# Optimization experiments

Measured on AMD Instinct MI355X. Metric: run time of the kernel, lower is better.

Reference implementation:

```python
import jax, jax.numpy as jnp
import numpy as np

FP8_MAX = 448.0  # max representable magnitude of float8_e4m3fn
SCALE_EPS = 1e-7


def setup_inputs() -> dict:
    key = jax.random.key(0)
    k1, k2, k3 = jax.random.split(key, 3)
    in_f, out_f = 2048, 2048
    x = jax.random.normal(k1, (4, 4096, in_f), dtype=jnp.float32)
    # weight is stored in fp8 in the torch module; materialize fp8-representable fp32 values
    w_fp32 = jax.random.normal(k2, (out_f, in_f), dtype=jnp.float32) * (1.0 / np.sqrt(in_f))
    weight = w_fp32.astype(jnp.float8_e4m3fn).astype(jnp.float32)
    weight_scale = jnp.ones((), dtype=jnp.float32)
    bound = 1.0 / np.sqrt(in_f)
    bias = jax.random.uniform(k3, (out_f,), dtype=jnp.float32, minval=-bound, maxval=bound)
    return {"x": x, "weight": weight, "weight_scale": weight_scale, "bias": bias}


def reference(x, weight, weight_scale, bias):
    # per-tensor dynamic fp8 quantization of the input (scale = absmax / 448)
    scale = jnp.maximum(jnp.max(jnp.abs(x)) / FP8_MAX, SCALE_EPS)
    x_q = (x / scale).astype(jnp.float8_e4m3fn).astype(jnp.float32)
    # dequantize weight (fp8 values stored as fp32 here) with its per-tensor scale
    w = weight * weight_scale
    # NOTE: faithful to the source, the output is NOT rescaled by the input scale
    # (the original forward drops input_scale after quantization).
    out = jnp.einsum('bsi,oi->bso', x_q, w) + bias
    return out
```

## Files before the change

### kernel.cpp

```cpp
#include <hip/hip_runtime.h>
#include <hip/hip_bf16.h>

typedef __attribute__((ext_vector_type(4))) float floatx4;
typedef __attribute__((ext_vector_type(8))) int   intx8;

#define FP8_MAX_F 448.0f
#define SCALE_EPS 1e-7f

__global__ void k_pre(const float* __restrict__ x, unsigned* __restrict__ amax, int n4,
                      const float* __restrict__ w, int* __restrict__ wq, int nw16) {
    if (blockIdx.x < 1792) {
        __shared__ float wmax[4];
        int tid = blockIdx.x * 256 + threadIdx.x;
        int stride = 1792 * 256;
        const float4* x4 = (const float4*)x;
        float m = 0.f;
        for (int i = tid; i < n4; i += stride) {
            float4 v = x4[i];
            m = fmaxf(fmaxf(fabsf(v.x), fabsf(v.y)),
                      fmaxf(m, fmaxf(fabsf(v.z), fabsf(v.w))));
        }
        #pragma unroll
        for (int off = 32; off > 0; off >>= 1) m = fmaxf(m, __shfl_xor(m, off, 64));
        if ((threadIdx.x & 63) == 0) wmax[threadIdx.x >> 6] = m;
        __syncthreads();
        if (threadIdx.x == 0) {
            float t = fmaxf(fmaxf(wmax[0], wmax[1]), fmaxf(wmax[2], wmax[3]));
            atomicMax(amax, __float_as_uint(t));
        }
    } else {
        int tid = (blockIdx.x - 1792) * 256 + threadIdx.x;
        int stride = 256 * 256;
        const float4* x4 = (const float4*)w;
        int4* q4 = (int4*)wq;
        for (int i = tid; i < nw16; i += stride) {
            float4 v0 = x4[4*i], v1 = x4[4*i+1], v2 = x4[4*i+2], v3 = x4[4*i+3];
            int4 o;
            o.x = __builtin_amdgcn_cvt_pk_fp8_f32(v0.x, v0.y, 0, false);
            o.x = __builtin_amdgcn_cvt_pk_fp8_f32(v0.z, v0.w, o.x, true);
            o.y = __builtin_amdgcn_cvt_pk_fp8_f32(v1.x, v1.y, 0, false);
            o.y = __builtin_amdgcn_cvt_pk_fp8_f32(v1.z, v1.w, o.y, true);
            o.z = __builtin_amdgcn_cvt_pk_fp8_f32(v2.x, v2.y, 0, false);
            o.z = __builtin_amdgcn_cvt_pk_fp8_f32(v2.z, v2.w, o.z, true);
            o.w = __builtin_amdgcn_cvt_pk_fp8_f32(v3.x, v3.y, 0, false);
            o.w = __builtin_amdgcn_cvt_pk_fp8_f32(v3.z, v3.w, o.w, true);
            q4[i] = o;
        }
    }
}

__global__ void k_quant_x(const float* __restrict__ x, int* __restrict__ xq,
                          const unsigned* __restrict__ amax, int n16) {
    float scale = fmaxf(__uint_as_float(*amax) / FP8_MAX_F, SCALE_EPS);
    int tid = blockIdx.x * blockDim.x + threadIdx.x;
    int stride = gridDim.x * blockDim.x;
    const float4* x4 = (const float4*)x;
    int4* q4 = (int4*)xq;
    for (int i = tid; i < n16; i += stride) {
        float4 v0 = x4[4*i], v1 = x4[4*i+1], v2 = x4[4*i+2], v3 = x4[4*i+3];
        int4 o;
        o.x = __builtin_amdgcn_cvt_pk_fp8_f32(v0.x / scale, v0.y / scale, 0, false);
        o.x = __builtin_amdgcn_cvt_pk_fp8_f32(v0.z / scale, v0.w / scale, o.x, true);
        o.y = __builtin_amdgcn_cvt_pk_fp8_f32(v1.x / scale, v1.y / scale, 0, false);
        o.y = __builtin_amdgcn_cvt_pk_fp8_f32(v1.z / scale, v1.w / scale, o.y, true);
        o.z = __builtin_amdgcn_cvt_pk_fp8_f32(v2.x / scale, v2.y / scale, 0, false);
        o.z = __builtin_amdgcn_cvt_pk_fp8_f32(v2.z / scale, v2.w / scale, o.z, true);
        o.w = __builtin_amdgcn_cvt_pk_fp8_f32(v3.x / scale, v3.y / scale, 0, false);
        o.w = __builtin_amdgcn_cvt_pk_fp8_f32(v3.z / scale, v3.w / scale, o.w, true);
        q4[i] = o;
    }
}

#define BM 256
#define BN 256
#define BKQ 128
#define NT 16

#define GLOAD(src, dst) \
    __builtin_amdgcn_global_load_lds((const __attribute__((address_space(1))) void*)(src), \
                                     (__attribute__((address_space(3))) void*)(dst), 16, 0, 0)
#define BARRIER()   asm volatile("s_barrier" ::: "memory")
#define WAIT_VM(n)  asm volatile("s_waitcnt vmcnt(" #n ")" ::: "memory")

#define LDFRAG(dstv, pL, pH, IMM) {                      \
    int4 lo_ = *(const int4*)((pL) + (IMM));             \
    int4 hi_ = *(const int4*)((pH) + (IMM));             \
    dstv = (intx8){lo_.x, lo_.y, lo_.z, lo_.w, hi_.x, hi_.y, hi_.z, hi_.w}; }

#define MFMA_ROW(m, af)                                                            \
    acc[m][0] = __builtin_amdgcn_mfma_scale_f32_16x16x128_f8f6f4(                  \
        af, b0, acc[m][0], 0, 0, 0, 0x7F7F7F7F, 0, 0x7F7F7F7F);                    \
    acc[m][1] = __builtin_amdgcn_mfma_scale_f32_16x16x128_f8f6f4(                  \
        af, b1, acc[m][1], 0, 0, 0, 0x7F7F7F7F, 0, 0x7F7F7F7F);                    \
    acc[m][2] = __builtin_amdgcn_mfma_scale_f32_16x16x128_f8f6f4(                  \
        af, b2, acc[m][2], 0, 0, 0, 0x7F7F7F7F, 0, 0x7F7F7F7F);                    \
    acc[m][3] = __builtin_amdgcn_mfma_scale_f32_16x16x128_f8f6f4(                  \
        af, b3, acc[m][3], 0, 0, 0, 0x7F7F7F7F, 0, 0x7F7F7F7F);

__global__ __launch_bounds__(512, 2) void k_gemm_mx(
    const unsigned char* __restrict__ A, const unsigned char* __restrict__ B,
    const float* __restrict__ bias, const float* __restrict__ wscale,
    float* __restrict__ C, int M, int N, int K) {
    __shared__ __align__(16) unsigned char lds[131072];

    int nwg = gridDim.x;
    int bid = blockIdx.x;
    bid = (bid & 7) * (nwg >> 3) + (bid >> 3);
    int ntn = N / BN;
    int tm = bid / ntn, tn = bid % ntn;
    int row0 = tm * BM, col0 = tn * BN;

    int tid = (int)threadIdx.x;
    int lane = tid & 63, wid = tid >> 6;
    int wr = wid >> 2, wc = wid & 3;
    int fr = lane & 15, g = lane >> 4;

    int srow = tid >> 3;
    int sc   = (tid & 7) ^ (srow & 7);
    const int offA0 = (row0 + srow) * K + sc * 16;
    const int offB0 = (col0 + srow) * K + sc * 16;
    unsigned char* dstA = lds + tid * 16;
    unsigned char* dstB = dstA + 32768;

    int c0 = (2 * g) ^ (fr & 7);
    const int aL = wr * 16384 + fr * 128 + c0 * 16;
    const int aH = wr * 16384 + fr * 128 + (c0 ^ 1) * 16;
    const int bL = 32768 + wc * 8192 + fr * 128 + c0 * 16;
    const int bH = 32768 + wc * 8192 + fr * 128 + (c0 ^ 1) * 16;

    floatx4 acc[8][4];
    #pragma unroll
    for (int m = 0; m < 8; ++m)
        #pragma unroll
        for (int n = 0; n < 4; ++n) acc[m][n] = (floatx4)(0.f);

    GLOAD(A + offA0,          dstA);
    GLOAD(A + offA0 + 131072, dstA + 8192);
    GLOAD(A + offA0 + 262144, dstA + 16384);
    GLOAD(A + offA0 + 393216, dstA + 24576);
    GLOAD(B + offB0,          dstB);
    GLOAD(B + offB0 + 131072, dstB + 8192);
    GLOAD(B + offB0 + 262144, dstB + 16384);
    GLOAD(B + offB0 + 393216, dstB + 24576);

    for (int t = 0; t < NT; ++t) {
        const int bufo = (t & 1) << 16;
        const int nbufo = bufo ^ 65536;
        const unsigned char* AbL = lds + bufo + aL;
        const unsigned char* AbH = lds + bufo + aH;
        const unsigned char* BbL = lds + bufo + bL;
        const unsigned char* BbH = lds + bufo + bH;
        unsigned char* dA = dstA + nbufo;
        unsigned char* dB = dstB + nbufo;
        const int kn = ((t + 1) & (NT - 1)) * BKQ;

        GLOAD(A + kn + offA0,          dA);
        GLOAD(A + kn + offA0 + 131072, dA + 8192);
        GLOAD(A + kn + offA0 + 262144, dA + 16384);
        GLOAD(A + kn + offA0 + 393216, dA + 24576);
        GLOAD(B + kn + offB0,          dB);
        GLOAD(B + kn + offB0 + 131072, dB + 8192);
        GLOAD(B + kn + offB0 + 262144, dB + 16384);
        GLOAD(B + kn + offB0 + 393216, dB + 24576);
        WAIT_VM(8);
        BARRIER();

        intx8 b0, b1, b2, b3, a0, a1, a2, a3, a4, a5, a6, a7;
        LDFRAG(b0, BbL, BbH, 0)
        LDFRAG(b1, BbL, BbH, 2048)
        LDFRAG(b2, BbL, BbH, 4096)
        LDFRAG(b3, BbL, BbH, 6144)
        LDFRAG(a0, AbL, AbH, 0)
        LDFRAG(a1, AbL, AbH, 2048)
        LDFRAG(a2, AbL, AbH, 4096)
        LDFRAG(a3, AbL, AbH, 6144)
        LDFRAG(a4, AbL, AbH, 8192)
        LDFRAG(a5, AbL, AbH, 10240)
        LDFRAG(a6, AbL, AbH, 12288)
        LDFRAG(a7, AbL, AbH, 14336)
        MFMA_ROW(0, a0)
        MFMA_ROW(1, a1)
        MFMA_ROW(2, a2)
        MFMA_ROW(3, a3)
        MFMA_ROW(4, a4)
        MFMA_ROW(5, a5)
        MFMA_ROW(6, a6)
        MFMA_ROW(7, a7)
        BARRIER();
    }

    WAIT_VM(0);

    float wsv = *wscale;
    int crow = (lane >> 4) * 4;
    int ccol = lane & 15;
    float bv[4];
    #pragma unroll
    for (int n = 0; n < 4; ++n) bv[n] = bias[col0 + wc * 64 + n * 16 + ccol];
    #pragma unroll
    for (int m = 0; m < 8; ++m) {
        int r = row0 + wr * 128 + m * 16 + crow;
        #pragma unroll
        for (int n = 0; n < 4; ++n) {
            int c = col0 + wc * 64 + n * 16 + ccol;
            #pragma unroll
            for (int j = 0; j < 4; ++j)
                C[(long)(r + j) * N + c] = acc[m][n][j] * wsv + bv[n];
        }
    }
}

extern "C" void kernel_launch(void* const* d_in, const int* in_sizes, int n_in,
                              void* d_out, int out_size, void* d_ws, size_t ws_size,
                              hipStream_t stream) {
    const float* x      = (const float*)d_in[0];
    const float* w      = (const float*)d_in[1];
    const float* wscale = (const float*)d_in[2];
    const float* bias   = (const float*)d_in[3];
    float* out = (float*)d_out;

    const int K = 2048, N = 2048;
    const int M = in_sizes[0] / K;

    unsigned char* ws = (unsigned char*)d_ws;
    unsigned* amax = (unsigned*)ws;
    int* wq = (int*)(ws + 1024);
    int* xq = (int*)(ws + 1024 + (size_t)N * K);

    hipMemsetAsync(amax, 0, 4, stream);
    k_pre<<<2048, 256, 0, stream>>>(x, amax, (M * K) / 4, w, wq, (N * K) / 16);
    k_quant_x<<<2048, 256, 0, stream>>>(x, xq, amax, (M * K) / 16);

    int grid = (M / BM) * (N / BN);
    k_gemm_mx<<<grid, 512, 0, stream>>>((const unsigned char*)xq, (const unsigned char*)wq,
                                        bias, wscale, out, M, N, K);
}
```

Measured before the change: 149.3 us.

## Load A operand directly from global into registers, stage only B in LDS

The GEMM main loop no longer stages the quantized A tile through LDS. Each wave now reads its A fragments straight from global memory into registers, and only B stays double-buffered in LDS, which halves the LDS allocation. The aim is to remove the A LDS write/read traffic and shrink the LDS footprint, and the MFMA block is wrapped in raised wave priority. The cost is that waves sharing the same row block fetch the same A data redundantly through the cache hierarchy. The A loads are also not prefetched a tile ahead, so their latency may be exposed every iteration.

```diff
diff --git a/kernel.cpp b/kernel.cpp
--- a/kernel.cpp
+++ b/kernel.cpp
@@ -79,12 +79,12 @@
 #define GLOAD(src, dst) \
     __builtin_amdgcn_global_load_lds((const __attribute__((address_space(1))) void*)(src), \
                                      (__attribute__((address_space(3))) void*)(dst), 16, 0, 0)
-#define BARRIER()   asm volatile("s_barrier" ::: "memory")
-#define WAIT_VM(n)  asm volatile("s_waitcnt vmcnt(" #n ")" ::: "memory")
-
-#define LDFRAG(dstv, pL, pH, IMM) {                      \
-    int4 lo_ = *(const int4*)((pL) + (IMM));             \
-    int4 hi_ = *(const int4*)((pH) + (IMM));             \
+#define BARRIER()    asm volatile("s_barrier" ::: "memory")
+#define WAIT_VM(n)   asm volatile("s_waitcnt vmcnt(" #n ")" ::: "memory")
+
+#define LDB(dstv, base, IMM) {                           \
+    int4 lo_ = *(const int4*)((base) + (IMM));           \
+    int4 hi_ = *(const int4*)((base) + 16 + (IMM));      \
     dstv = (intx8){lo_.x, lo_.y, lo_.z, lo_.w, hi_.x, hi_.y, hi_.z, hi_.w}; }
 
 #define MFMA_ROW(m, af)                                                            \
@@ -101,7 +101,7 @@
     const unsigned char* __restrict__ A, const unsigned char* __restrict__ B,
     const float* __restrict__ bias, const float* __restrict__ wscale,
     float* __restrict__ C, int M, int N, int K) {
-    __shared__ __align__(16) unsigned char lds[131072];
+    __shared__ __align__(16) unsigned char lds[65536];
 
     int nwg = gridDim.x;
     int bid = blockIdx.x;
@@ -117,16 +117,14 @@
 
     int srow = tid >> 3;
     int sc   = (tid & 7) ^ (srow & 7);
-    const int offA0 = (row0 + srow) * K + sc * 16;
     const int offB0 = (col0 + srow) * K + sc * 16;
-    unsigned char* dstA = lds + tid * 16;
-    unsigned char* dstB = dstA + 32768;
+    unsigned char* dstB = lds + tid * 16;
 
     int c0 = (2 * g) ^ (fr & 7);
-    const int aL = wr * 16384 + fr * 128 + c0 * 16;
-    const int aH = wr * 16384 + fr * 128 + (c0 ^ 1) * 16;
-    const int bL = 32768 + wc * 8192 + fr * 128 + c0 * 16;
-    const int bH = 32768 + wc * 8192 + fr * 128 + (c0 ^ 1) * 16;
+    const int bL = wc * 8192 + fr * 128 + c0 * 16;
+    const int bH = wc * 8192 + fr * 128 + (c0 ^ 1) * 16;
+
+    const int aBase = (row0 + wr * 128 + fr) * K + g * 32;
 
     floatx4 acc[8][4];
     #pragma unroll
@@ -134,50 +132,54 @@
         #pragma unroll
         for (int n = 0; n < 4; ++n) acc[m][n] = (floatx4)(0.f);
 
-    GLOAD(A + offA0,          dstA);
-    GLOAD(A + offA0 + 131072, dstA + 8192);
-    GLOAD(A + offA0 + 262144, dstA + 16384);
-    GLOAD(A + offA0 + 393216, dstA + 24576);
     GLOAD(B + offB0,          dstB);
     GLOAD(B + offB0 + 131072, dstB + 8192);
     GLOAD(B + offB0 + 262144, dstB + 16384);
     GLOAD(B + offB0 + 393216, dstB + 24576);
 
     for (int t = 0; t < NT; ++t) {
-        const int bufo = (t & 1) << 16;
-        const int nbufo = bufo ^ 65536;
-        const unsigned char* AbL = lds + bufo + aL;
-        const unsigned char* AbH = lds + bufo + aH;
+        const int bufo = (t & 1) << 15;
         const unsigned char* BbL = lds + bufo + bL;
         const unsigned char* BbH = lds + bufo + bH;
-        unsigned char* dA = dstA + nbufo;
-        unsigned char* dB = dstB + nbufo;
+        unsigned char* dB = dstB + (bufo ^ 32768);
+        const int kt = t * BKQ;
         const int kn = ((t + 1) & (NT - 1)) * BKQ;
 
-        GLOAD(A + kn + offA0,          dA);
-        GLOAD(A + kn + offA0 + 131072, dA + 8192);
-        GLOAD(A + kn + offA0 + 262144, dA + 16384);
-        GLOAD(A + kn + offA0 + 393216, dA + 24576);
+        intx8 a0, a1, a2, a3, a4, a5, a6, a7;
+        const unsigned char* Ap = A + aBase + kt;
+        LDB(a0, Ap, 0)
+        LDB(a1, Ap, 32768)
+        LDB(a2, Ap, 65536)
+        LDB(a3, Ap, 98304)
+        LDB(a4, Ap, 131072)
+        LDB(a5, Ap, 163840)
+        LDB(a6, Ap, 196608)
+        LDB(a7, Ap, 229376)
+
         GLOAD(B + kn + offB0,          dB);
         GLOAD(B + kn + offB0 + 131072, dB + 8192);
         GLOAD(B + kn + offB0 + 262144, dB + 16384);
         GLOAD(B + kn + offB0 + 393216, dB + 24576);
-        WAIT_VM(8);
+
+        WAIT_VM(4);
         BARRIER();
 
-        intx8 b0, b1, b2, b3, a0, a1, a2, a3, a4, a5, a6, a7;
-        LDFRAG(b0, BbL, BbH, 0)
-        LDFRAG(b1, BbL, BbH, 2048)
-        LDFRAG(b2, BbL, BbH, 4096)
-        LDFRAG(b3, BbL, BbH, 6144)
-        LDFRAG(a0, AbL, AbH, 0)
-        LDFRAG(a1, AbL, AbH, 2048)
-        LDFRAG(a2, AbL, AbH, 4096)
-        LDFRAG(a3, AbL, AbH, 6144)
-        LDFRAG(a4, AbL, AbH, 8192)
-        LDFRAG(a5, AbL, AbH, 10240)
-        LDFRAG(a6, AbL, AbH, 12288)
-        LDFRAG(a7, AbL, AbH, 14336)
+        intx8 b0, b1, b2, b3;
+        {
+            int4 lo0 = *(const int4*)(BbL + 0);
+            int4 hi0 = *(const int4*)(BbH + 0);
+            int4 lo1 = *(const int4*)(BbL + 2048);
+            int4 hi1 = *(const int4*)(BbH + 2048);
+            int4 lo2 = *(const int4*)(BbL + 4096);
+            int4 hi2 = *(const int4*)(BbH + 4096);
+            int4 lo3 = *(const int4*)(BbL + 6144);
+            int4 hi3 = *(const int4*)(BbH + 6144);
+            b0 = (intx8){lo0.x, lo0.y, lo0.z, lo0.w, hi0.x, hi0.y, hi0.z, hi0.w};
+            b1 = (intx8){lo1.x, lo1.y, lo1.z, lo1.w, hi1.x, hi1.y, hi1.z, hi1.w};
+            b2 = (intx8){lo2.x, lo2.y, lo2.z, lo2.w, hi2.x, hi2.y, hi2.z, hi2.w};
+            b3 = (intx8){lo3.x, lo3.y, lo3.z, lo3.w, hi3.x, hi3.y, hi3.z, hi3.w};
+        }
+        __builtin_amdgcn_s_setprio(1);
         MFMA_ROW(0, a0)
         MFMA_ROW(1, a1)
         MFMA_ROW(2, a2)
@@ -186,6 +188,7 @@
         MFMA_ROW(5, a5)
         MFMA_ROW(6, a6)
         MFMA_ROW(7, a7)
+        __builtin_amdgcn_s_setprio(0);
         BARRIER();
     }
 
```

After: 251.8 us. 1.69x slower.
